# Kernel optimization log

Hardware: AMD Instinct MI355X
Metric: run time of the kernel (lower is better)

The kernel has to match this reference:

```python
import jax, jax.numpy as jnp
import numpy as np

T, DIM, HID = 8192, 1024, 4096

def setup_inputs() -> dict:
    key = jax.random.key(0)
    k1, k2, k3 = jax.random.split(key, 3)
    x = jax.random.normal(k1, (T, DIM), dtype=jnp.float32)
    # torch Linear weight layout: [out_features, in_features]
    W_fc = jax.random.normal(k2, (HID, DIM), dtype=jnp.float32) * 0.02
    W_proj = jax.random.normal(k3, (DIM, HID), dtype=jnp.float32) * 0.02
    return {"x": x, "W_fc": W_fc, "W_proj": W_proj}

def reference(x, W_fc, W_proj):
    # fc: x @ W_fc^T  -> relu -> square -> proj: @ W_proj^T
    h = jnp.einsum('td,hd->th', x, W_fc)      # [T, HID]
    h = jnp.square(jax.nn.relu(h))            # relu(h)^2 (relu^2 activation)
    return jnp.einsum('th,dh->td', h, W_proj) # [T, DIM]
```

## Files before the change

kernel.cpp:

```cpp
#include <hip/hip_runtime.h>
#include <stdint.h>


#define BM 128
#define BN 128
#define BK 64

typedef __attribute__((ext_vector_type(8))) short bf16x8;
typedef __attribute__((ext_vector_type(4))) float f32x4;

typedef const __attribute__((address_space(1))) unsigned int* gas_u32p;
typedef __attribute__((address_space(3))) unsigned int* las_u32p;

__device__ __forceinline__ void load16_to_lds(const void* gptr, void* lptr) {
    __builtin_amdgcn_global_load_lds((gas_u32p)gptr, (las_u32p)lptr, 16, 0, 0);
}

__device__ __forceinline__ unsigned short f2bf(float f) {
    unsigned int u = __float_as_uint(f);
    u += 0x7FFFu + ((u >> 16) & 1u);
    return (unsigned short)(u >> 16);
}

__global__ void cvt_all(const float4* __restrict__ x,  ushort4* __restrict__ xb,
                        const float4* __restrict__ wf, ushort4* __restrict__ wfb,
                        const float4* __restrict__ wp, ushort4* __restrict__ wpb)
{
    const int base = blockIdx.x * 1024 + threadIdx.x;
    #pragma unroll
    for (int j = 0; j < 4; j++) {
        const int i = base + j * 256;
        const float4* s; ushort4* d; int k;
        if (i < (1 << 21))            { s = x;  d = xb;  k = i; }
        else if (i < 3 * (1 << 20))   { s = wf; d = wfb; k = i - (1 << 21); }
        else                          { s = wp; d = wpb; k = i - 3 * (1 << 20); }
        float4 v = s[k];
        ushort4 o;
        o.x = f2bf(v.x); o.y = f2bf(v.y); o.z = f2bf(v.z); o.w = f2bf(v.w);
        d[k] = o;
    }
}

template<bool RELU2, bool OUT_BF16>
__global__ __launch_bounds__(256, 3)
void gemm_bt(const unsigned short* __restrict__ A,
             const unsigned short* __restrict__ B,
             void* __restrict__ Cv, int M, int N, int K)
{
    __shared__ unsigned short sA[BM * BK];
    __shared__ unsigned short sB[BN * BK];

    const int tid  = threadIdx.x;
    const int lane = tid & 63;
    const int wave = tid >> 6;
    const int wm   = (wave >> 1) * 64;
    const int wn   = (wave & 1) * 64;
    const int quad = lane >> 4;
    const int m16  = lane & 15;

    const long bm0 = (long)blockIdx.y * BM;
    const long bn0 = (long)blockIdx.x * BN;

    const int srow = tid >> 3;
    const int scol = (tid & 7) * 8;

    const unsigned short* gA = A + (bm0 + srow) * (long)K + scol;
    const unsigned short* gB = B + (bn0 + srow) * (long)K + scol;
    char* lA = (char*)sA + tid * 16;
    char* lB = (char*)sB + tid * 16;

    f32x4 acc[4][4];
    #pragma unroll
    for (int i = 0; i < 4; i++)
        #pragma unroll
        for (int j = 0; j < 4; j++)
            acc[i][j] = (f32x4)0.0f;

    for (int k0 = 0; k0 < K; k0 += BK) {
        #pragma unroll
        for (int c = 0; c < 4; c++)
            load16_to_lds(gA + (long)c * 32 * K + k0, lA + c * 4096);
        #pragma unroll
        for (int c = 0; c < 4; c++)
            load16_to_lds(gB + (long)c * 32 * K + k0, lB + c * 4096);
        __syncthreads();

        #pragma unroll
        for (int h = 0; h < 2; h++) {
            bf16x8 af[4], bfr[4];
            #pragma unroll
            for (int i = 0; i < 4; i++)
                af[i]  = *(const bf16x8*)&sA[(wm + i * 16 + m16) * BK + h * 32 + quad * 8];
            #pragma unroll
            for (int j = 0; j < 4; j++)
                bfr[j] = *(const bf16x8*)&sB[(wn + j * 16 + m16) * BK + h * 32 + quad * 8];

            #pragma unroll
            for (int i = 0; i < 4; i++)
                #pragma unroll
                for (int j = 0; j < 4; j++)
                    acc[i][j] = __builtin_amdgcn_mfma_f32_16x16x32_bf16(
                        af[i], bfr[j], acc[i][j], 0, 0, 0);
        }
        __syncthreads();
    }

    #pragma unroll
    for (int i = 0; i < 4; i++) {
        #pragma unroll
        for (int j = 0; j < 4; j++) {
            #pragma unroll
            for (int r = 0; r < 4; r++) {
                float v = acc[i][j][r];
                if (RELU2) v = (v > 0.0f) ? v * v : 0.0f;
                const long row = bm0 + wm + i * 16 + quad * 4 + r;
                const long col = bn0 + wn + j * 16 + m16;
                if (OUT_BF16)
                    ((unsigned short*)Cv)[row * (long)N + col] = f2bf(v);
                else
                    ((float*)Cv)[row * (long)N + col] = v;
            }
        }
    }
}

extern "C" void kernel_launch(void* const* d_in, const int* in_sizes, int n_in,
                              void* d_out, int out_size, void* d_ws, size_t ws_size,
                              hipStream_t stream) {
    (void)in_sizes; (void)n_in; (void)out_size; (void)ws_size;

    const int T = 8192, DIM = 1024, HID = 4096;

    const float* x     = (const float*)d_in[0];
    const float* W_fc  = (const float*)d_in[1];
    const float* W_prj = (const float*)d_in[2];
    float* out = (float*)d_out;

    char* ws = (char*)d_ws;
    unsigned short* h   = (unsigned short*)ws;
    unsigned short* xb  = (unsigned short*)(ws + (64l << 20));
    unsigned short* wfb = (unsigned short*)(ws + (80l << 20));
    unsigned short* wpb = (unsigned short*)(ws + (88l << 20));

    cvt_all<<<4096, 256, 0, stream>>>(
        (const float4*)x,     (ushort4*)xb,
        (const float4*)W_fc,  (ushort4*)wfb,
        (const float4*)W_prj, (ushort4*)wpb);

    gemm_bt<true, true><<<dim3(HID / BN, T / BM), dim3(256), 0, stream>>>(
        xb, wfb, h, T, HID, DIM);

    gemm_bt<false, false><<<dim3(DIM / BN, T / BM), dim3(256), 0, stream>>>(
        h, wpb, out, T, DIM, HID);
}
```

Baseline: 272.7 us.

## Enlarge GEMM tiles to 256-wide with 8 waves and simplify conversion dispatch

The GEMM kernel becomes templated on block tile and wave grid, and launches with 512 threads. The first GEMM uses 256x256 tiles and the second uses 256x128 tiles, which raises data reuse per LDS tile and cuts global traffic. The conversion kernel now picks its source array once per block instead of once per element. Larger tiles increase register and LDS pressure, lower occupancy, and leave fewer blocks to spread across the CUs (512 and 256 blocks).

```diff
diff --git a/kernel.cpp b/kernel.cpp
--- a/kernel.cpp
+++ b/kernel.cpp
@@ -2,8 +2,6 @@
 #include <stdint.h>
 
 
-#define BM 128
-#define BN 128
 #define BK 64
 
 typedef __attribute__((ext_vector_type(8))) short bf16x8;
@@ -22,39 +20,47 @@
     return (unsigned short)(u >> 16);
 }
 
-__global__ void cvt_all(const float4* __restrict__ x,  ushort4* __restrict__ xb,
-                        const float4* __restrict__ wf, ushort4* __restrict__ wfb,
-                        const float4* __restrict__ wp, ushort4* __restrict__ wpb)
+__global__ __launch_bounds__(256)
+void cvt_all(const float4* __restrict__ x,  ushort4* __restrict__ xb,
+             const float4* __restrict__ wf, ushort4* __restrict__ wfb,
+             const float4* __restrict__ wp, ushort4* __restrict__ wpb)
 {
-    const int base = blockIdx.x * 1024 + threadIdx.x;
+    const int b = blockIdx.x;
+    const float4* s; ushort4* d; int base;
+    if (b < 2048)      { s = x;  d = xb;  base = b * 1024; }
+    else if (b < 3072) { s = wf; d = wfb; base = (b - 2048) * 1024; }
+    else               { s = wp; d = wpb; base = (b - 3072) * 1024; }
+    const int i0 = base + threadIdx.x;
     #pragma unroll
     for (int j = 0; j < 4; j++) {
-        const int i = base + j * 256;
-        const float4* s; ushort4* d; int k;
-        if (i < (1 << 21))            { s = x;  d = xb;  k = i; }
-        else if (i < 3 * (1 << 20))   { s = wf; d = wfb; k = i - (1 << 21); }
-        else                          { s = wp; d = wpb; k = i - 3 * (1 << 20); }
-        float4 v = s[k];
+        float4 v = s[i0 + j * 256];
         ushort4 o;
         o.x = f2bf(v.x); o.y = f2bf(v.y); o.z = f2bf(v.z); o.w = f2bf(v.w);
-        d[k] = o;
+        d[i0 + j * 256] = o;
     }
 }
 
-template<bool RELU2, bool OUT_BF16>
-__global__ __launch_bounds__(256, 3)
+template<int BM, int BN, int NWM, int NWN, bool RELU2, bool OUT_BF16>
+__global__ __launch_bounds__(512, 2)
 void gemm_bt(const unsigned short* __restrict__ A,
              const unsigned short* __restrict__ B,
              void* __restrict__ Cv, int M, int N, int K)
 {
+    constexpr int WR = BM / NWM;
+    constexpr int WC = BN / NWN;
+    constexpr int AI = WR / 16;
+    constexpr int AJ = WC / 16;
+    constexpr int CA = BM / 64;
+    constexpr int CB = BN / 64;
+
     __shared__ unsigned short sA[BM * BK];
     __shared__ unsigned short sB[BN * BK];
 
     const int tid  = threadIdx.x;
     const int lane = tid & 63;
     const int wave = tid >> 6;
-    const int wm   = (wave >> 1) * 64;
-    const int wn   = (wave & 1) * 64;
+    const int wmr  = (wave / NWN) * WR;
+    const int wnc  = (wave % NWN) * WC;
     const int quad = lane >> 4;
     const int m16  = lane & 15;
 
@@ -69,36 +75,36 @@
     char* lA = (char*)sA + tid * 16;
     char* lB = (char*)sB + tid * 16;
 
-    f32x4 acc[4][4];
+    f32x4 acc[AI][AJ];
     #pragma unroll
-    for (int i = 0; i < 4; i++)
+    for (int i = 0; i < AI; i++)
         #pragma unroll
-        for (int j = 0; j < 4; j++)
+        for (int j = 0; j < AJ; j++)
             acc[i][j] = (f32x4)0.0f;
 
     for (int k0 = 0; k0 < K; k0 += BK) {
         #pragma unroll
-        for (int c = 0; c < 4; c++)
-            load16_to_lds(gA + (long)c * 32 * K + k0, lA + c * 4096);
+        for (int c = 0; c < CA; c++)
+            load16_to_lds(gA + (long)c * 64 * K + k0, lA + c * 8192);
         #pragma unroll
-        for (int c = 0; c < 4; c++)
-            load16_to_lds(gB + (long)c * 32 * K + k0, lB + c * 4096);
+        for (int c = 0; c < CB; c++)
+            load16_to_lds(gB + (long)c * 64 * K + k0, lB + c * 8192);
         __syncthreads();
 
         #pragma unroll
         for (int h = 0; h < 2; h++) {
-            bf16x8 af[4], bfr[4];
+            bf16x8 af[AI], bfr[AJ];
             #pragma unroll
-            for (int i = 0; i < 4; i++)
-                af[i]  = *(const bf16x8*)&sA[(wm + i * 16 + m16) * BK + h * 32 + quad * 8];
+            for (int i = 0; i < AI; i++)
+                af[i]  = *(const bf16x8*)&sA[(wmr + i * 16 + m16) * BK + h * 32 + quad * 8];
             #pragma unroll
-            for (int j = 0; j < 4; j++)
-                bfr[j] = *(const bf16x8*)&sB[(wn + j * 16 + m16) * BK + h * 32 + quad * 8];
+            for (int j = 0; j < AJ; j++)
+                bfr[j] = *(const bf16x8*)&sB[(wnc + j * 16 + m16) * BK + h * 32 + quad * 8];
 
             #pragma unroll
-            for (int i = 0; i < 4; i++)
+            for (int i = 0; i < AI; i++)
                 #pragma unroll
-                for (int j = 0; j < 4; j++)
+                for (int j = 0; j < AJ; j++)
                     acc[i][j] = __builtin_amdgcn_mfma_f32_16x16x32_bf16(
                         af[i], bfr[j], acc[i][j], 0, 0, 0);
         }
@@ -106,15 +112,15 @@
     }
 
     #pragma unroll
-    for (int i = 0; i < 4; i++) {
+    for (int i = 0; i < AI; i++) {
         #pragma unroll
-        for (int j = 0; j < 4; j++) {
+        for (int j = 0; j < AJ; j++) {
             #pragma unroll
             for (int r = 0; r < 4; r++) {
                 float v = acc[i][j][r];
                 if (RELU2) v = (v > 0.0f) ? v * v : 0.0f;
-                const long row = bm0 + wm + i * 16 + quad * 4 + r;
-                const long col = bn0 + wn + j * 16 + m16;
+                const long row = bm0 + wmr + i * 16 + quad * 4 + r;
+                const long col = bn0 + wnc + j * 16 + m16;
                 if (OUT_BF16)
                     ((unsigned short*)Cv)[row * (long)N + col] = f2bf(v);
                 else
@@ -147,9 +153,11 @@
         (const float4*)W_fc,  (ushort4*)wfb,
         (const float4*)W_prj, (ushort4*)wpb);
 
-    gemm_bt<true, true><<<dim3(HID / BN, T / BM), dim3(256), 0, stream>>>(
-        xb, wfb, h, T, HID, DIM);
+    gemm_bt<256, 256, 2, 4, true, true>
+        <<<dim3(HID / 256, T / 256), dim3(512), 0, stream>>>(
+            xb, wfb, h, T, HID, DIM);
 
-    gemm_bt<false, false><<<dim3(DIM / BN, T / BM), dim3(256), 0, stream>>>(
-        h, wpb, out, T, DIM, HID);
+    gemm_bt<256, 128, 4, 2, false, false>
+        <<<dim3(DIM / 128, T / 256), dim3(512), 0, stream>>>(
+            h, wpb, out, T, DIM, HID);
 }
```

New measurement: 332.8 us. 1.22x slower.
